# Performance work log

Hardware: AMD Instinct MI355X
Metric: run time of the kernel (lower is better)

The kernel has to match this reference:

```python
import jax, jax.numpy as jnp
import numpy as np


def _topk_gate(v, k):
    # keep values >= k-th largest (ties kept, matching torch semantics)
    topk_vals = jax.lax.top_k(v, k)[0]          # (B, k)
    thr = topk_vals[:, -1:]                      # (B, 1)
    return v * (v >= thr).astype(v.dtype)


def setup_inputs() -> dict:
    key = jax.random.key(0)
    ks = jax.random.split(key, 12)
    B, S, D, R, M = 8, 2048, 1024, 64, 256
    H = 4 * D
    def lin(k, fan_out, fan_in):
        bound = 1.0 / np.sqrt(fan_in)
        return jax.random.uniform(k, (fan_out, fan_in), jnp.float32, -bound, bound)
    def bias(k, fan_out, fan_in):
        bound = 1.0 / np.sqrt(fan_in)
        return jax.random.uniform(k, (fan_out,), jnp.float32, -bound, bound)
    return {
        "x": jax.random.normal(ks[0], (B, S, D), jnp.float32),
        "state": jnp.zeros((B, M), jnp.float32),
        "U_w": lin(ks[1], R, D),
        "V_w": lin(ks[2], R, D),
        "w1": lin(ks[3], H, D),
        "b1": bias(ks[4], H, D),
        "w2": lin(ks[5], D, H),
        "b2": bias(ks[6], D, H),
        "win_w": lin(ks[7], M, D),
        "win_b": bias(ks[8], M, D),
        "wstate": lin(ks[9], M, M),
        "gamma": jnp.float32(0.9),
        "top_k": 32,
    }


def reference(x, state, U_w, V_w, w1, b1, w2, b2, win_w, win_b, wstate, gamma, top_k):
    # outputs depend only on x (residual + FFN), computed vectorized over seq.
    h = jax.nn.relu(jnp.einsum("bsd,hd->bsh", x, w1) + b1)
    outputs = x + jnp.einsum("bsh,dh->bsd", h, w2) + b2   # (B, S, D)
    # Note: U_proj / V_proj are computed but unused in the original forward
    # (dead code); omitted here as they do not affect outputs or memory.

    # precompute W_in projection for all timesteps: (B, S, M)
    x_proj = jnp.einsum("bsd,md->bsm", x, win_w) + win_b

    def step(carry, xp_t):
        st, mem = carry
        su = jax.nn.relu(st @ wstate.T + xp_t)            # (B, M)
        g = _topk_gate(su, top_k)
        mem = gamma * mem + (1.0 - gamma) * g
        return (g, mem), None

    (_, memory), _ = jax.lax.scan(step, (state, state), jnp.swapaxes(x_proj, 0, 1))
    return outputs, memory
```

## Files before the change

kernel.cpp:

```cpp
#include <hip/hip_runtime.h>
#include <stdint.h>

#define BB 8
#define SS 2048
#define DD 1024
#define HH 4096
#define MM 256

typedef short bf16x8 __attribute__((ext_vector_type(8)));
typedef float f32x4 __attribute__((ext_vector_type(4)));

__device__ inline unsigned short f2bf(float f){
  unsigned u = __builtin_bit_cast(unsigned, f);
  return (unsigned short)((u + 0x7FFFu + ((u >> 16) & 1u)) >> 16);
}

__global__ void ssma_pack_bf16(const float* __restrict__ src,
                               unsigned short* __restrict__ dst, int n4){
  int i = blockIdx.x * blockDim.x + threadIdx.x;
  if (i < n4){
    float4 v = ((const float4*)src)[i];
    ushort4 o;
    o.x = f2bf(v.x); o.y = f2bf(v.y); o.z = f2bf(v.z); o.w = f2bf(v.w);
    ((ushort4*)dst)[i] = o;
  }
}

template<int EPI>
__global__ __launch_bounds__(256) void ssma_gemm_bt(
    const unsigned short* __restrict__ A, const unsigned short* __restrict__ Bw,
    int K, int N, const float* __restrict__ bias,
    const float* __restrict__ resid, void* __restrict__ Cout)
{
  __shared__ uint4 As4[512];
  __shared__ uint4 Bs4[512];
  unsigned short* As = (unsigned short*)As4;
  unsigned short* Bs = (unsigned short*)Bs4;

  const int tid  = threadIdx.x;
  const int lane = tid & 63;
  const int wv   = tid >> 6;
  const int wm   = wv >> 1, wn = wv & 1;
  const int m0   = blockIdx.y * 128;
  const int n0   = blockIdx.x * 128;
  const int kq   = lane >> 4;
  const int rl   = lane & 15;

  f32x4 acc[4][4];
#pragma unroll
  for (int a = 0; a < 4; ++a)
#pragma unroll
    for (int b = 0; b < 4; ++b) acc[a][b] = (f32x4){0.f, 0.f, 0.f, 0.f};

  for (int k0 = 0; k0 < K; k0 += 32){
    __syncthreads();
#pragma unroll
    for (int i = 0; i < 2; ++i){
      int c  = tid + 256 * i;
      int r  = c >> 2;
      int c8 = (c & 3) * 8;
      As4[c] = *(const uint4*)(A  + (size_t)(m0 + r) * K + k0 + c8);
      Bs4[c] = *(const uint4*)(Bw + (size_t)(n0 + r) * K + k0 + c8);
    }
    __syncthreads();

    const bf16x8* Ap = (const bf16x8*)As;
    const bf16x8* Bp = (const bf16x8*)Bs;
    bf16x8 af[4], bfr[4];
#pragma unroll
    for (int mi = 0; mi < 4; ++mi) af[mi]  = Ap[(wm * 64 + mi * 16 + rl) * 4 + kq];
#pragma unroll
    for (int ni = 0; ni < 4; ++ni) bfr[ni] = Bp[(wn * 64 + ni * 16 + rl) * 4 + kq];
#pragma unroll
    for (int mi = 0; mi < 4; ++mi)
#pragma unroll
      for (int ni = 0; ni < 4; ++ni)
        acc[mi][ni] = __builtin_amdgcn_mfma_f32_16x16x32_bf16(af[mi], bfr[ni], acc[mi][ni], 0, 0, 0);
  }

#pragma unroll
  for (int mi = 0; mi < 4; ++mi){
#pragma unroll
    for (int ni = 0; ni < 4; ++ni){
      int col = n0 + wn * 64 + ni * 16 + rl;
      float bv = bias[col];
#pragma unroll
      for (int r = 0; r < 4; ++r){
        int row = m0 + wm * 64 + mi * 16 + kq * 4 + r;
        float v = acc[mi][ni][r] + bv;
        if (EPI == 0){
          v = fmaxf(v, 0.0f);
          ((unsigned short*)Cout)[(size_t)row * N + col] = f2bf(v);
        } else {
          v += resid[(size_t)row * N + col];
          ((float*)Cout)[(size_t)row * N + col] = v;
        }
      }
    }
  }
}

__global__ __launch_bounds__(256) void ssma_gemm3_f32(
    const float* __restrict__ A, const float* __restrict__ Bw,
    const float* __restrict__ bias, float* __restrict__ C)
{
  __shared__ float As[64][17];
  __shared__ float Bs[64][17];
  const int tid = threadIdx.x;
  const int tx = tid & 15, ty = tid >> 4;
  const int m0 = blockIdx.y * 64, n0 = blockIdx.x * 64;
  float acc[4][4];
#pragma unroll
  for (int i = 0; i < 4; ++i)
#pragma unroll
    for (int j = 0; j < 4; ++j) acc[i][j] = 0.f;

  for (int k0 = 0; k0 < DD; k0 += 16){
    __syncthreads();
#pragma unroll
    for (int i = 0; i < 4; ++i){
      int e = tid + 256 * i;
      int r = e >> 4, c = e & 15;
      As[r][c] = A [(size_t)(m0 + r) * DD + k0 + c];
      Bs[r][c] = Bw[(size_t)(n0 + r) * DD + k0 + c];
    }
    __syncthreads();
#pragma unroll
    for (int kk = 0; kk < 16; ++kk){
      float a[4], b[4];
#pragma unroll
      for (int i = 0; i < 4; ++i) a[i] = As[ty * 4 + i][kk];
#pragma unroll
      for (int j = 0; j < 4; ++j) b[j] = Bs[tx * 4 + j][kk];
#pragma unroll
      for (int i = 0; i < 4; ++i)
#pragma unroll
        for (int j = 0; j < 4; ++j) acc[i][j] = fmaf(a[i], b[j], acc[i][j]);
    }
  }
#pragma unroll
  for (int i = 0; i < 4; ++i){
    int row = m0 + ty * 4 + i;
#pragma unroll
    for (int j = 0; j < 4; ++j){
      int col = n0 + tx * 4 + j;
      C[(size_t)row * MM + col] = acc[i][j] + bias[col];
    }
  }
}

__global__ __launch_bounds__(256) void ssma_transpose(
    const float* __restrict__ A, float* __restrict__ At)
{
  __shared__ float t[32][33];
  const int tx = threadIdx.x & 31, ty = threadIdx.x >> 5;
  const int x0 = blockIdx.x * 32, y0 = blockIdx.y * 32;
#pragma unroll
  for (int r = 0; r < 32; r += 8)
    t[ty + r][tx] = A[(size_t)(y0 + ty + r) * MM + x0 + tx];
  __syncthreads();
#pragma unroll
  for (int r = 0; r < 32; r += 8)
    At[(size_t)(x0 + ty + r) * MM + y0 + tx] = t[tx][ty + r];
}

__global__ __launch_bounds__(1024, 4) void ssma_scan6(
    const float* __restrict__ xproj, const float* __restrict__ state,
    const float* __restrict__ wT, const float* __restrict__ gamma_p,
    const int* __restrict__ topk_p, float* __restrict__ mem_out)
{
  __shared__ __align__(16) int   kidx[MM + 32];
  __shared__ __align__(16) float kval[MM + 32];
  __shared__ __align__(16) unsigned long long umask[4];
  __shared__ __align__(16) int   hist[256];
  __shared__ __align__(16) int   suf_gt[256];
  __shared__ __align__(16) float cand[256];
  __shared__ int ccnt;

  const int tid  = threadIdx.x;
  const int wv   = tid >> 6;
  const int lane = tid & 63;
  const int b    = blockIdx.x;
  const float gamma = *gamma_p;
  const float omg   = 1.0f - gamma;
  const int   K     = *topk_p;

  const float* xp  = xproj + (size_t)b * SS * MM;
  const float* wTm = wT + tid;

  if (tid < 64) ((int4*)hist)[tid] = (int4){0, 0, 0, 0};
  if (tid == 1023) ccnt = 0;

  float mem = 0.0f, st0 = 0.0f;
  if (tid < MM){
    st0 = state[b * MM + tid];
    mem = st0;
    unsigned long long pmi = __ballot(st0 != 0.0f);
    if (lane == 0) umask[wv] = pmi;
  }
  __syncthreads();
  int nkp;
  {
    unsigned long long u0 = umask[0], u1 = umask[1], u2 = umask[2], u3 = umask[3];
    int nk = __popcll(u0) + __popcll(u1) + __popcll(u2) + __popcll(u3);
    if (tid < MM && st0 != 0.0f){
      int before = (wv > 0 ? __popcll(u0) : 0) + (wv > 1 ? __popcll(u1) : 0)
                 + (wv > 2 ? __popcll(u2) : 0);
      unsigned long long mw = (wv == 0 ? u0 : wv == 1 ? u1 : wv == 2 ? u2 : u3);
      int pos = before + __popcll(mw & ((1ull << lane) - 1ull));
      kidx[pos] = tid << 8;
      kval[pos] = st0;
    }
    nkp = (nk + 15) & ~15; if (nkp < 32) nkp = 32;
    if (tid >= MM && tid < MM + 64){
      int t2 = tid - MM;
      if (nk + t2 < nkp){ kidx[nk + t2] = 0; kval[nk + t2] = 0.0f; }
    }
  }
  float xp_cur = (tid < MM) ? xp[tid] : 0.0f;
  __syncthreads();

  for (int t = 0; t < SS; ++t){
    float su = 0.0f, xp_next = 0.0f;
    int bin = 0;
    if (tid < MM){
      int tn = (t + 1 < SS) ? t + 1 : SS - 1;
      xp_next = xp[(size_t)tn * MM + tid];

      const int4*   ip = (const int4*)kidx;
      const float4* vp = (const float4*)kval;
      int4   I[8];
      float4 V[8];
#pragma unroll
      for (int j = 0; j < 8; ++j){ I[j] = ip[j]; V[j] = vp[j]; }
      float a0=0.f,a1=0.f,a2=0.f,a3=0.f,a4=0.f,a5=0.f,a6=0.f,a7=0.f;
      float w00=wTm[I[0].x], w01=wTm[I[0].y], w02=wTm[I[0].z], w03=wTm[I[0].w];
      float w10=wTm[I[1].x], w11=wTm[I[1].y], w12=wTm[I[1].z], w13=wTm[I[1].w];
      float w20=wTm[I[2].x], w21=wTm[I[2].y], w22=wTm[I[2].z], w23=wTm[I[2].w];
      float w30=wTm[I[3].x], w31=wTm[I[3].y], w32=wTm[I[3].z], w33=wTm[I[3].w];
      float w40=wTm[I[4].x], w41=wTm[I[4].y], w42=wTm[I[4].z], w43=wTm[I[4].w];
      float w50=wTm[I[5].x], w51=wTm[I[5].y], w52=wTm[I[5].z], w53=wTm[I[5].w];
      float w60=wTm[I[6].x], w61=wTm[I[6].y], w62=wTm[I[6].z], w63=wTm[I[6].w];
      float w70=wTm[I[7].x], w71=wTm[I[7].y], w72=wTm[I[7].z], w73=wTm[I[7].w];
      a0=fmaf(w00,V[0].x,a0); a0=fmaf(w01,V[0].y,a0); a0=fmaf(w02,V[0].z,a0); a0=fmaf(w03,V[0].w,a0);
      a1=fmaf(w10,V[1].x,a1); a1=fmaf(w11,V[1].y,a1); a1=fmaf(w12,V[1].z,a1); a1=fmaf(w13,V[1].w,a1);
      a2=fmaf(w20,V[2].x,a2); a2=fmaf(w21,V[2].y,a2); a2=fmaf(w22,V[2].z,a2); a2=fmaf(w23,V[2].w,a2);
      a3=fmaf(w30,V[3].x,a3); a3=fmaf(w31,V[3].y,a3); a3=fmaf(w32,V[3].z,a3); a3=fmaf(w33,V[3].w,a3);
      a4=fmaf(w40,V[4].x,a4); a4=fmaf(w41,V[4].y,a4); a4=fmaf(w42,V[4].z,a4); a4=fmaf(w43,V[4].w,a4);
      a5=fmaf(w50,V[5].x,a5); a5=fmaf(w51,V[5].y,a5); a5=fmaf(w52,V[5].z,a5); a5=fmaf(w53,V[5].w,a5);
      a6=fmaf(w60,V[6].x,a6); a6=fmaf(w61,V[6].y,a6); a6=fmaf(w62,V[6].z,a6); a6=fmaf(w63,V[6].w,a6);
      a7=fmaf(w70,V[7].x,a7); a7=fmaf(w71,V[7].y,a7); a7=fmaf(w72,V[7].z,a7); a7=fmaf(w73,V[7].w,a7);
      if (nkp > 32){
        for (int c4 = 8; c4 < (nkp >> 2); ++c4){
          int4 I2 = ip[c4]; float4 V2 = vp[c4];
          a0 = fmaf(wTm[I2.x], V2.x, a0); a1 = fmaf(wTm[I2.y], V2.y, a1);
          a2 = fmaf(wTm[I2.z], V2.z, a2); a3 = fmaf(wTm[I2.w], V2.w, a3);
        }
      }
      float s = ((a0 + a1) + (a2 + a3)) + ((a4 + a5) + (a6 + a7));
      su = fmaxf(s + xp_cur, 0.0f);
      if (su > 0.0f){
        bin = (int)(__float_as_uint(su) >> 23);
        atomicAdd(&hist[bin], 1);
      }
    }
    __syncthreads();

    if (tid < 64){
      int4 h4 = ((const int4*)hist)[tid];
      int t4 = h4.x + h4.y + h4.z + h4.w;
      int I = t4;
#pragma unroll
      for (int off = 1; off < 64; off <<= 1){
        int x = __shfl_down(I, off);
        I += (lane + off < 64) ? x : 0;
      }
      int E = I - t4;
      int4 s4;
      s4.w = E;
      s4.z = E + h4.w;
      s4.y = s4.z + h4.z;
      s4.x = s4.y + h4.y;
      ((int4*)suf_gt)[tid] = s4;
    }
    __syncthreads();

    float g = 0.0f;
    int   a = 0;
    bool  bound = false;
    if (tid < MM && su > 0.0f){
      a = suf_gt[bin];
      int hb = hist[bin];
      if (a >= K)            g = 0.0f;
      else if (a + hb <= K)  g = su;
      else { bound = true; int p = atomicAdd(&ccnt, 1); cand[p] = su; }
    }
    __syncthreads();

    if (bound){
      int C = __builtin_amdgcn_readfirstlane(ccnt);
      int w = 0;
      for (int j = 0; j < C; ++j) w += (cand[j] > su);
      g = (a + w <= K - 1) ? su : 0.0f;
    }
    if (tid < MM){
      mem = fmaf(gamma, mem, omg * g);
      unsigned long long pm = __ballot(g > 0.0f);
      if (lane == 0) umask[wv] = pm;
    }
    __syncthreads();

    {
      unsigned long long u0 = umask[0], u1 = umask[1], u2 = umask[2], u3 = umask[3];
      int nk = __popcll(u0) + __popcll(u1) + __popcll(u2) + __popcll(u3);
      if (tid < MM && g > 0.0f){
        int before = (wv > 0 ? __popcll(u0) : 0) + (wv > 1 ? __popcll(u1) : 0)
                   + (wv > 2 ? __popcll(u2) : 0);
        unsigned long long mw = (wv == 0 ? u0 : wv == 1 ? u1 : wv == 2 ? u2 : u3);
        int pos = before + __popcll(mw & ((1ull << lane) - 1ull));
        kidx[pos] = tid << 8;
        kval[pos] = g;
      }
      nkp = (nk + 15) & ~15; if (nkp < 32) nkp = 32;
      if (tid >= MM && tid < MM + 64){
        int t2 = tid - MM;
        if (nk + t2 < nkp){ kidx[nk + t2] = 0; kval[nk + t2] = 0.0f; }
      }
      if (tid >= 512 && tid < 576) ((int4*)hist)[tid - 512] = (int4){0, 0, 0, 0};
      if (tid == 1023) ccnt = 0;
    }
    xp_cur = xp_next;
    __syncthreads();
  }
  if (tid < MM) mem_out[b * MM + tid] = mem;
}

extern "C" void kernel_launch(void* const* d_in, const int* in_sizes, int n_in,
                              void* d_out, int out_size, void* d_ws, size_t ws_size,
                              hipStream_t stream)
{
  const float* x      = (const float*)d_in[0];
  const float* state  = (const float*)d_in[1];
  const float* w1     = (const float*)d_in[4];
  const float* b1     = (const float*)d_in[5];
  const float* w2     = (const float*)d_in[6];
  const float* b2     = (const float*)d_in[7];
  const float* win_w  = (const float*)d_in[8];
  const float* win_b  = (const float*)d_in[9];
  const float* wstate = (const float*)d_in[10];
  const float* gammap = (const float*)d_in[11];
  const int*   topkp  = (const int*)d_in[12];

  float* out  = (float*)d_out;
  float* memo = out + (size_t)BB * SS * DD;

  char* ws = (char*)d_ws;
  unsigned short* xb   = (unsigned short*)(ws);
  unsigned short* w1b  = (unsigned short*)(ws + 33554432);
  unsigned short* w2b  = (unsigned short*)(ws + 41943040);
  unsigned short* hbuf = (unsigned short*)(ws + 50331648);
  float*          xprj = (float*)(ws + 184549376);
  float*          wT   = (float*)(ws + 33554432);

  ssma_pack_bf16<<<16384, 256, 0, stream>>>(x,  xb,  4194304);
  ssma_pack_bf16<<<4096,  256, 0, stream>>>(w1, w1b, 1048576);
  ssma_pack_bf16<<<4096,  256, 0, stream>>>(w2, w2b, 1048576);

  ssma_gemm3_f32<<<dim3(4, 256), 256, 0, stream>>>(x, win_w, win_b, xprj);

  ssma_gemm_bt<0><<<dim3(32, 128), 256, 0, stream>>>(xb, w1b, 1024, 4096, b1, nullptr, (void*)hbuf);

  ssma_transpose<<<dim3(8, 8), 256, 0, stream>>>(wstate, wT);

  ssma_gemm_bt<1><<<dim3(8, 128), 256, 0, stream>>>(hbuf, w2b, 4096, 1024, b2, x, (void*)out);

  ssma_scan6<<<BB, 1024, 0, stream>>>(xprj, state, wT, gammap, topkp, memo);
}
```

Baseline: 6.007 ms.

## Fuse FFN GEMMs and sequential top-k scan into one persistent concurrent kernel

Merges the two FFN GEMMs and the recurrent top-k scan into a single launch. Eight blocks run the latency-bound scan while 248 persistent worker blocks process the GEMM tiles concurrently, with a global atomic counter acting as a grid barrier between GEMM1 and GEMM2. The scan is also reworked to use 256 threads with a 64-bin exponent histogram, a wave-shuffle prefix sum and ds_bpermute lookups, and a ballot-based tie resolution, which removes several block-wide barriers per step. Possible downsides are deadlock if not all 256 blocks are co-resident, fewer GEMM workers than before, and contention between the scan blocks and the GEMMs for CU resources.

```diff
diff --git a/kernel.cpp b/kernel.cpp
--- a/kernel.cpp
+++ b/kernel.cpp
@@ -6,6 +6,7 @@
 #define DD 1024
 #define HH 4096
 #define MM 256
+#define NWORK 248
 
 typedef short bf16x8 __attribute__((ext_vector_type(8)));
 typedef float f32x4 __attribute__((ext_vector_type(4)));
@@ -27,22 +28,20 @@
 }
 
 template<int EPI>
-__global__ __launch_bounds__(256) void ssma_gemm_bt(
-    const unsigned short* __restrict__ A, const unsigned short* __restrict__ Bw,
-    int K, int N, const float* __restrict__ bias,
-    const float* __restrict__ resid, void* __restrict__ Cout)
-{
-  __shared__ uint4 As4[512];
-  __shared__ uint4 Bs4[512];
+__device__ void gemm_tile(const unsigned short* __restrict__ A,
+                          const unsigned short* __restrict__ Bw,
+                          int K, int N, const float* __restrict__ bias,
+                          const float* __restrict__ resid, void* __restrict__ Cout,
+                          int bx, int by, uint4* As4, uint4* Bs4)
+{
   unsigned short* As = (unsigned short*)As4;
   unsigned short* Bs = (unsigned short*)Bs4;
-
   const int tid  = threadIdx.x;
   const int lane = tid & 63;
   const int wv   = tid >> 6;
   const int wm   = wv >> 1, wn = wv & 1;
-  const int m0   = blockIdx.y * 128;
-  const int n0   = blockIdx.x * 128;
+  const int m0   = by * 128;
+  const int n0   = bx * 128;
   const int kq   = lane >> 4;
   const int rl   = lane & 15;
 
@@ -98,6 +97,7 @@
       }
     }
   }
+  __syncthreads();
 }
 
 __global__ __launch_bounds__(256) void ssma_gemm3_f32(
@@ -164,23 +164,47 @@
     At[(size_t)(x0 + ty + r) * MM + y0 + tx] = t[tx][ty + r];
 }
 
-__global__ __launch_bounds__(1024, 4) void ssma_scan6(
+__global__ __launch_bounds__(256, 2) void ssma_fused(
     const float* __restrict__ xproj, const float* __restrict__ state,
     const float* __restrict__ wT, const float* __restrict__ gamma_p,
-    const int* __restrict__ topk_p, float* __restrict__ mem_out)
-{
+    const int* __restrict__ topk_p, float* __restrict__ mem_out,
+    const unsigned short* __restrict__ xb, const unsigned short* __restrict__ w1b,
+    const unsigned short* __restrict__ w2b, unsigned short* __restrict__ hbuf,
+    const float* __restrict__ b1, const float* __restrict__ b2,
+    const float* __restrict__ xres, float* __restrict__ out,
+    unsigned int* __restrict__ ctr)
+{
+  __shared__ uint4 As4[512];
+  __shared__ uint4 Bs4[512];
+  __shared__ __align__(16) float su_all[MM];
+  __shared__ __align__(16) int   hist[64];
   __shared__ __align__(16) int   kidx[MM + 32];
   __shared__ __align__(16) float kval[MM + 32];
   __shared__ __align__(16) unsigned long long umask[4];
-  __shared__ __align__(16) int   hist[256];
-  __shared__ __align__(16) int   suf_gt[256];
-  __shared__ __align__(16) float cand[256];
-  __shared__ int ccnt;
-
-  const int tid  = threadIdx.x;
+  __shared__ __align__(16) unsigned long long bmask[4];
+
+  const int tid = threadIdx.x;
+
+  if (blockIdx.x >= 8){
+    const int wid = blockIdx.x - 8;
+    for (int t = wid; t < 4096; t += NWORK)
+      gemm_tile<0>(xb, w1b, 1024, 4096, b1, nullptr, (void*)hbuf, t & 31, t >> 5, As4, Bs4);
+    if (tid == 0){
+      __threadfence();
+      atomicAdd(ctr, 1u);
+      while (__hip_atomic_load(ctr, __ATOMIC_RELAXED, __HIP_MEMORY_SCOPE_AGENT) < NWORK)
+        __builtin_amdgcn_s_sleep(32);
+    }
+    __syncthreads();
+    __threadfence();
+    for (int t = wid; t < 1024; t += NWORK)
+      gemm_tile<1>(hbuf, w2b, 4096, 1024, b2, xres, (void*)out, t & 7, t >> 3, As4, Bs4);
+    return;
+  }
+
+  const int b    = blockIdx.x;
   const int wv   = tid >> 6;
   const int lane = tid & 63;
-  const int b    = blockIdx.x;
   const float gamma = *gamma_p;
   const float omg   = 1.0f - gamma;
   const int   K     = *topk_p;
@@ -188,13 +212,11 @@
   const float* xp  = xproj + (size_t)b * SS * MM;
   const float* wTm = wT + tid;
 
-  if (tid < 64) ((int4*)hist)[tid] = (int4){0, 0, 0, 0};
-  if (tid == 1023) ccnt = 0;
-
-  float mem = 0.0f, st0 = 0.0f;
-  if (tid < MM){
-    st0 = state[b * MM + tid];
-    mem = st0;
+  if (tid < 16) ((int4*)hist)[tid] = (int4){0, 0, 0, 0};
+
+  float mem = state[b * MM + tid];
+  float st0 = mem;
+  {
     unsigned long long pmi = __ballot(st0 != 0.0f);
     if (lane == 0) umask[wv] = pmi;
   }
@@ -203,7 +225,7 @@
   {
     unsigned long long u0 = umask[0], u1 = umask[1], u2 = umask[2], u3 = umask[3];
     int nk = __popcll(u0) + __popcll(u1) + __popcll(u2) + __popcll(u3);
-    if (tid < MM && st0 != 0.0f){
+    if (st0 != 0.0f){
       int before = (wv > 0 ? __popcll(u0) : 0) + (wv > 1 ? __popcll(u1) : 0)
                  + (wv > 2 ? __popcll(u2) : 0);
       unsigned long long mw = (wv == 0 ? u0 : wv == 1 ? u1 : wv == 2 ? u2 : u3);
@@ -211,100 +233,97 @@
       kidx[pos] = tid << 8;
       kval[pos] = st0;
     }
-    nkp = (nk + 15) & ~15; if (nkp < 32) nkp = 32;
-    if (tid >= MM && tid < MM + 64){
-      int t2 = tid - MM;
-      if (nk + t2 < nkp){ kidx[nk + t2] = 0; kval[nk + t2] = 0.0f; }
-    }
-  }
-  float xp_cur = (tid < MM) ? xp[tid] : 0.0f;
+    nkp = (nk + 3) & ~3; if (nkp < 32) nkp = 32;
+    if (tid < 64 && nk + tid < nkp){ kidx[nk + tid] = 0; kval[nk + tid] = 0.0f; }
+  }
+  float xp_cur = xp[tid];
   __syncthreads();
 
   for (int t = 0; t < SS; ++t){
-    float su = 0.0f, xp_next = 0.0f;
+    int tn = (t + 1 < SS) ? t + 1 : SS - 1;
+    float xp_next = xp[(size_t)tn * MM + tid];
+
+    const int4*   ip = (const int4*)kidx;
+    const float4* vp = (const float4*)kval;
+    int4   I[8];
+    float4 V[8];
+#pragma unroll
+    for (int j = 0; j < 8; ++j){ I[j] = ip[j]; V[j] = vp[j]; }
+    float a0=0.f,a1=0.f,a2=0.f,a3=0.f,a4=0.f,a5=0.f,a6=0.f,a7=0.f;
+    float w00=wTm[I[0].x], w01=wTm[I[0].y], w02=wTm[I[0].z], w03=wTm[I[0].w];
+    float w10=wTm[I[1].x], w11=wTm[I[1].y], w12=wTm[I[1].z], w13=wTm[I[1].w];
+    float w20=wTm[I[2].x], w21=wTm[I[2].y], w22=wTm[I[2].z], w23=wTm[I[2].w];
+    float w30=wTm[I[3].x], w31=wTm[I[3].y], w32=wTm[I[3].z], w33=wTm[I[3].w];
+    float w40=wTm[I[4].x], w41=wTm[I[4].y], w42=wTm[I[4].z], w43=wTm[I[4].w];
+    float w50=wTm[I[5].x], w51=wTm[I[5].y], w52=wTm[I[5].z], w53=wTm[I[5].w];
+    float w60=wTm[I[6].x], w61=wTm[I[6].y], w62=wTm[I[6].z], w63=wTm[I[6].w];
+    float w70=wTm[I[7].x], w71=wTm[I[7].y], w72=wTm[I[7].z], w73=wTm[I[7].w];
+    a0=fmaf(w00,V[0].x,a0); a0=fmaf(w01,V[0].y,a0); a0=fmaf(w02,V[0].z,a0); a0=fmaf(w03,V[0].w,a0);
+    a1=fmaf(w10,V[1].x,a1); a1=fmaf(w11,V[1].y,a1); a1=fmaf(w12,V[1].z,a1); a1=fmaf(w13,V[1].w,a1);
+    a2=fmaf(w20,V[2].x,a2); a2=fmaf(w21,V[2].y,a2); a2=fmaf(w22,V[2].z,a2); a2=fmaf(w23,V[2].w,a2);
+    a3=fmaf(w30,V[3].x,a3); a3=fmaf(w31,V[3].y,a3); a3=fmaf(w32,V[3].z,a3); a3=fmaf(w33,V[3].w,a3);
+    a4=fmaf(w40,V[4].x,a4); a4=fmaf(w41,V[4].y,a4); a4=fmaf(w42,V[4].z,a4); a4=fmaf(w43,V[4].w,a4);
+    a5=fmaf(w50,V[5].x,a5); a5=fmaf(w51,V[5].y,a5); a5=fmaf(w52,V[5].z,a5); a5=fmaf(w53,V[5].w,a5);
+    a6=fmaf(w60,V[6].x,a6); a6=fmaf(w61,V[6].y,a6); a6=fmaf(w62,V[6].z,a6); a6=fmaf(w63,V[6].w,a6);
+    a7=fmaf(w70,V[7].x,a7); a7=fmaf(w71,V[7].y,a7); a7=fmaf(w72,V[7].z,a7); a7=fmaf(w73,V[7].w,a7);
+    if (nkp > 32){
+      for (int c4 = 8; c4 < (nkp >> 2); ++c4){
+        int4 I2 = ip[c4]; float4 V2 = vp[c4];
+        a0 = fmaf(wTm[I2.x], V2.x, a0); a1 = fmaf(wTm[I2.y], V2.y, a1);
+        a2 = fmaf(wTm[I2.z], V2.z, a2); a3 = fmaf(wTm[I2.w], V2.w, a3);
+      }
+    }
+    float s = ((a0 + a1) + (a2 + a3)) + ((a4 + a5) + (a6 + a7));
+    float su = fmaxf(s + xp_cur, 0.0f);
+    su_all[tid] = su;
+
     int bin = 0;
-    if (tid < MM){
-      int tn = (t + 1 < SS) ? t + 1 : SS - 1;
-      xp_next = xp[(size_t)tn * MM + tid];
-
-      const int4*   ip = (const int4*)kidx;
-      const float4* vp = (const float4*)kval;
-      int4   I[8];
-      float4 V[8];
-#pragma unroll
-      for (int j = 0; j < 8; ++j){ I[j] = ip[j]; V[j] = vp[j]; }
-      float a0=0.f,a1=0.f,a2=0.f,a3=0.f,a4=0.f,a5=0.f,a6=0.f,a7=0.f;
-      float w00=wTm[I[0].x], w01=wTm[I[0].y], w02=wTm[I[0].z], w03=wTm[I[0].w];
-      float w10=wTm[I[1].x], w11=wTm[I[1].y], w12=wTm[I[1].z], w13=wTm[I[1].w];
-      float w20=wTm[I[2].x], w21=wTm[I[2].y], w22=wTm[I[2].z], w23=wTm[I[2].w];
-      float w30=wTm[I[3].x], w31=wTm[I[3].y], w32=wTm[I[3].z], w33=wTm[I[3].w];
-      float w40=wTm[I[4].x], w41=wTm[I[4].y], w42=wTm[I[4].z], w43=wTm[I[4].w];
-      float w50=wTm[I[5].x], w51=wTm[I[5].y], w52=wTm[I[5].z], w53=wTm[I[5].w];
-      float w60=wTm[I[6].x], w61=wTm[I[6].y], w62=wTm[I[6].z], w63=wTm[I[6].w];
-      float w70=wTm[I[7].x], w71=wTm[I[7].y], w72=wTm[I[7].z], w73=wTm[I[7].w];
-      a0=fmaf(w00,V[0].x,a0); a0=fmaf(w01,V[0].y,a0); a0=fmaf(w02,V[0].z,a0); a0=fmaf(w03,V[0].w,a0);
-      a1=fmaf(w10,V[1].x,a1); a1=fmaf(w11,V[1].y,a1); a1=fmaf(w12,V[1].z,a1); a1=fmaf(w13,V[1].w,a1);
-      a2=fmaf(w20,V[2].x,a2); a2=fmaf(w21,V[2].y,a2); a2=fmaf(w22,V[2].z,a2); a2=fmaf(w23,V[2].w,a2);
-      a3=fmaf(w30,V[3].x,a3); a3=fmaf(w31,V[3].y,a3); a3=fmaf(w32,V[3].z,a3); a3=fmaf(w33,V[3].w,a3);
-      a4=fmaf(w40,V[4].x,a4); a4=fmaf(w41,V[4].y,a4); a4=fmaf(w42,V[4].z,a4); a4=fmaf(w43,V[4].w,a4);
-      a5=fmaf(w50,V[5].x,a5); a5=fmaf(w51,V[5].y,a5); a5=fmaf(w52,V[5].z,a5); a5=fmaf(w53,V[5].w,a5);
-      a6=fmaf(w60,V[6].x,a6); a6=fmaf(w61,V[6].y,a6); a6=fmaf(w62,V[6].z,a6); a6=fmaf(w63,V[6].w,a6);
-      a7=fmaf(w70,V[7].x,a7); a7=fmaf(w71,V[7].y,a7); a7=fmaf(w72,V[7].z,a7); a7=fmaf(w73,V[7].w,a7);
-      if (nkp > 32){
-        for (int c4 = 8; c4 < (nkp >> 2); ++c4){
-          int4 I2 = ip[c4]; float4 V2 = vp[c4];
-          a0 = fmaf(wTm[I2.x], V2.x, a0); a1 = fmaf(wTm[I2.y], V2.y, a1);
-          a2 = fmaf(wTm[I2.z], V2.z, a2); a3 = fmaf(wTm[I2.w], V2.w, a3);
+    if (su > 0.0f){
+      int e = (int)(__float_as_uint(su) >> 23);
+      bin = e - 0x58; bin = bin < 0 ? 0 : (bin > 63 ? 63 : bin);
+      atomicAdd(&hist[bin], 1);
+    }
+    __syncthreads();
+
+    int h = hist[lane];
+    int inc = h;
+#pragma unroll
+    for (int off = 1; off < 64; off <<= 1){
+      int xv = __shfl_down(inc, off);
+      inc += (lane + off < 64) ? xv : 0;
+    }
+    int E = inc - h;
+    int a  = __builtin_amdgcn_ds_bpermute(bin << 2, E);
+    int hb = __builtin_amdgcn_ds_bpermute(bin << 2, h);
+
+    float g = 0.0f;
+    bool bnd = false;
+    if (su > 0.0f){
+      if (a >= K)            g = 0.0f;
+      else if (a + hb <= K)  g = su;
+      else                   bnd = true;
+    }
+    {
+      unsigned long long bm = __ballot(bnd);
+      if (lane == 0) bmask[wv] = bm;
+    }
+    __syncthreads();
+
+    if (bnd){
+      int w = 0;
+#pragma unroll
+      for (int w4 = 0; w4 < 4; ++w4){
+        unsigned long long u = bmask[w4];
+        while (u){
+          int j = __ffsll((long long)u) - 1;
+          u &= u - 1;
+          w += (su_all[w4 * 64 + j] > su);
         }
       }
-      float s = ((a0 + a1) + (a2 + a3)) + ((a4 + a5) + (a6 + a7));
-      su = fmaxf(s + xp_cur, 0.0f);
-      if (su > 0.0f){
-        bin = (int)(__float_as_uint(su) >> 23);
-        atomicAdd(&hist[bin], 1);
-      }
-    }
-    __syncthreads();
-
-    if (tid < 64){
-      int4 h4 = ((const int4*)hist)[tid];
-      int t4 = h4.x + h4.y + h4.z + h4.w;
-      int I = t4;
-#pragma unroll
-      for (int off = 1; off < 64; off <<= 1){
-        int x = __shfl_down(I, off);
-        I += (lane + off < 64) ? x : 0;
-      }
-      int E = I - t4;
-      int4 s4;
-      s4.w = E;
-      s4.z = E + h4.w;
-      s4.y = s4.z + h4.z;
-      s4.x = s4.y + h4.y;
-      ((int4*)suf_gt)[tid] = s4;
-    }
-    __syncthreads();
-
-    float g = 0.0f;
-    int   a = 0;
-    bool  bound = false;
-    if (tid < MM && su > 0.0f){
-      a = suf_gt[bin];
-      int hb = hist[bin];
-      if (a >= K)            g = 0.0f;
-      else if (a + hb <= K)  g = su;
-      else { bound = true; int p = atomicAdd(&ccnt, 1); cand[p] = su; }
-    }
-    __syncthreads();
-
-    if (bound){
-      int C = __builtin_amdgcn_readfirstlane(ccnt);
-      int w = 0;
-      for (int j = 0; j < C; ++j) w += (cand[j] > su);
       g = (a + w <= K - 1) ? su : 0.0f;
     }
-    if (tid < MM){
-      mem = fmaf(gamma, mem, omg * g);
+    mem = fmaf(gamma, mem, omg * g);
+    {
       unsigned long long pm = __ballot(g > 0.0f);
       if (lane == 0) umask[wv] = pm;
     }
@@ -313,7 +332,7 @@
     {
       unsigned long long u0 = umask[0], u1 = umask[1], u2 = umask[2], u3 = umask[3];
       int nk = __popcll(u0) + __popcll(u1) + __popcll(u2) + __popcll(u3);
-      if (tid < MM && g > 0.0f){
+      if (g > 0.0f){
         int before = (wv > 0 ? __popcll(u0) : 0) + (wv > 1 ? __popcll(u1) : 0)
                    + (wv > 2 ? __popcll(u2) : 0);
         unsigned long long mw = (wv == 0 ? u0 : wv == 1 ? u1 : wv == 2 ? u2 : u3);
@@ -321,18 +340,14 @@
         kidx[pos] = tid << 8;
         kval[pos] = g;
       }
-      nkp = (nk + 15) & ~15; if (nkp < 32) nkp = 32;
-      if (tid >= MM && tid < MM + 64){
-        int t2 = tid - MM;
-        if (nk + t2 < nkp){ kidx[nk + t2] = 0; kval[nk + t2] = 0.0f; }
-      }
-      if (tid >= 512 && tid < 576) ((int4*)hist)[tid - 512] = (int4){0, 0, 0, 0};
-      if (tid == 1023) ccnt = 0;
+      nkp = (nk + 3) & ~3; if (nkp < 32) nkp = 32;
+      if (tid < 64 && nk + tid < nkp){ kidx[nk + tid] = 0; kval[nk + tid] = 0.0f; }
+      if (tid >= 64 && tid < 80) ((int4*)hist)[tid - 64] = (int4){0, 0, 0, 0};
     }
     xp_cur = xp_next;
     __syncthreads();
   }
-  if (tid < MM) mem_out[b * MM + tid] = mem;
+  mem_out[b * MM + tid] = mem;
 }
 
 extern "C" void kernel_launch(void* const* d_in, const int* in_sizes, int n_in,
@@ -360,19 +375,19 @@
   unsigned short* w2b  = (unsigned short*)(ws + 41943040);
   unsigned short* hbuf = (unsigned short*)(ws + 50331648);
   float*          xprj = (float*)(ws + 184549376);
-  float*          wT   = (float*)(ws + 33554432);
+  float*          wT   = (float*)(ws + 201326592);
+  unsigned int*   ctr  = (unsigned int*)(ws + 201326592 + 262144);
 
   ssma_pack_bf16<<<16384, 256, 0, stream>>>(x,  xb,  4194304);
   ssma_pack_bf16<<<4096,  256, 0, stream>>>(w1, w1b, 1048576);
   ssma_pack_bf16<<<4096,  256, 0, stream>>>(w2, w2b, 1048576);
 
   ssma_gemm3_f32<<<dim3(4, 256), 256, 0, stream>>>(x, win_w, win_b, xprj);
-
-  ssma_gemm_bt<0><<<dim3(32, 128), 256, 0, stream>>>(xb, w1b, 1024, 4096, b1, nullptr, (void*)hbuf);
-
   ssma_transpose<<<dim3(8, 8), 256, 0, stream>>>(wstate, wT);
 
-  ssma_gemm_bt<1><<<dim3(8, 128), 256, 0, stream>>>(hbuf, w2b, 4096, 1024, b2, x, (void*)out);
-
-  ssma_scan6<<<BB, 1024, 0, stream>>>(xprj, state, wT, gammap, topkp, memo);
-}
+  hipMemsetAsync(ctr, 0, 8, stream);
+
+  ssma_fused<<<8 + NWORK, 256, 0, stream>>>(
+      xprj, state, wT, gammap, topkp, memo,
+      xb, w1b, w2b, hbuf, b1, b2, x, out, ctr);
+}
```

New measurement: 8.224 ms. +36.9%, slower.
